# Kernel optimization log

Measured on AMD Instinct MI355X. Metric: run time of the kernel, lower is better.

The kernel has to match this reference:

```python
import jax, jax.numpy as jnp
import numpy as np
import math

INPUT_DIM = 1024
QUERY_DIM = 1024
VALUE_DIM = 1024

def setup_inputs() -> dict:
    key = jax.random.key(0)
    ks = jax.random.split(key, 7)
    N, T, D = 4, 4096, INPUT_DIM
    s_in = 1.0 / math.sqrt(D)
    X = jax.random.normal(ks[0], (N, T, D), dtype=jnp.float32)
    # torch.nn.Linear weights: (out, in), init ~ U(-1/sqrt(in), 1/sqrt(in))
    Wq = jax.random.uniform(ks[1], (QUERY_DIM, D), jnp.float32, -s_in, s_in)
    bq = jax.random.uniform(ks[2], (QUERY_DIM,), jnp.float32, -s_in, s_in)
    Wk = jax.random.uniform(ks[3], (QUERY_DIM, D), jnp.float32, -s_in, s_in)
    bk = jax.random.uniform(ks[4], (QUERY_DIM,), jnp.float32, -s_in, s_in)
    Wv = jax.random.uniform(ks[5], (VALUE_DIM, D), jnp.float32, -s_in, s_in)
    bv = jax.random.uniform(ks[6], (VALUE_DIM,), jnp.float32, -s_in, s_in)
    return {"X": X, "Wq": Wq, "bq": bq, "Wk": Wk, "bk": bk, "Wv": Wv, "bv": bv}

def reference(X, Wq, bq, Wk, bk, Wv, bv):
    N, T, D = X.shape
    q = jnp.einsum('ntd,qd->ntq', X, Wq) + bq  # (N,T,Q)
    k = jnp.einsum('ntd,qd->ntq', X, Wk) + bk  # (N,T,Q)
    v = jnp.einsum('ntd,vd->ntv', X, Wv) + bv  # (N,T,V)
    # NOTE: original scales by sqrt(D) = sqrt(input_dim), not sqrt(query_dim)
    scores = jnp.einsum('ntq,nsq->nts', q, k) / jnp.sqrt(jnp.asarray(D, X.dtype))
    attn = jax.nn.softmax(scores, axis=-1)  # (N,T,T)
    return jnp.einsum('nts,nsv->ntv', attn, v)
```

## Files before the change

kernel.cpp:

```cpp
#include <hip/hip_runtime.h>
#include <stdint.h>

typedef unsigned short u16;
typedef unsigned int u32;
typedef short shortx8 __attribute__((ext_vector_type(8)));
typedef float floatx4 __attribute__((ext_vector_type(4)));

__device__ __forceinline__ u16 f2bf(float f) {
    u32 u = __builtin_bit_cast(u32, f);
    u = (u + 0x7fffu + ((u >> 16) & 1u)) >> 16;
    return (u16)u;
}
__device__ __forceinline__ float bf2f(u16 h) {
    return __builtin_bit_cast(float, (u32)h << 16);
}

#if defined(__has_builtin)
#  if __has_builtin(__builtin_amdgcn_global_load_lds)
#    define HAVE_GLL 1
#  endif
#endif
#ifndef HAVE_GLL
#  define HAVE_GLL 0
#endif

#if HAVE_GLL
__device__ __forceinline__ void gload_lds16(const u16* g, u16* l) {
    __builtin_amdgcn_global_load_lds(
        (const __attribute__((address_space(1))) u32*)(const void*)g,
        (__attribute__((address_space(3))) u32*)(void*)l,
        16, 0, 0);
}
#endif

template <typename OutT, int MODE, int SWZ>
__global__ __launch_bounds__(256, 2) void gemm_bt(
    const u16* __restrict__ Ag, const u16* __restrict__ Bg, OutT* __restrict__ Cg,
    int lda, int ldb, int ldc, int K,
    const float* __restrict__ aux, float* __restrict__ sums, float scale,
    long long sAz, long long sBz, long long sCz, long long sXz,
    int swz_nhalf)
{
    __shared__ u16 smem[4][128 * 32];

    int z, mb, nb;
    if constexpr (SWZ) {
        const int f = blockIdx.x, xcd = f & 7, g = f >> 3;
        z = xcd >> 1;
        mb = g & 31;
        nb = (xcd & 1) * swz_nhalf + (g >> 5);
    } else {
        z = blockIdx.z; mb = blockIdx.y; nb = blockIdx.x;
    }
    const int m0 = mb * 128, n0 = nb * 128;

    const u16* A = Ag + (long long)z * sAz;
    const u16* B = Bg + (long long)z * sBz;
    OutT* C = Cg + (long long)z * sCz;
    const float* auxp = nullptr;
    if constexpr (MODE == 1 || MODE == 2 || MODE == 4)
        auxp = aux + (long long)z * sXz;
    float* sumz = nullptr;
    if constexpr (MODE == 3) sumz = sums + (long long)z * sXz;

    const int tid = threadIdx.x, lane = tid & 63, wv = tid >> 6;

    const int srow = lane >> 2;
    const int schunk = (lane & 3) * 8;
    const u16* gA0 = A + (size_t)(m0 + wv * 16 + srow) * lda + schunk;
    const u16* gA1 = gA0 + (size_t)64 * lda;
    const u16* gB0 = B + (size_t)(n0 + wv * 16 + srow) * ldb + schunk;
    const u16* gB1 = gB0 + (size_t)64 * ldb;
    const int wb = wv * 512;

    const int wm = (wv & 1) * 64, wn = (wv >> 1) * 64;
    const int mi = lane & 15, kq = lane >> 4;

    floatx4 acc[4][4] = {};

    for (int k0 = 0; k0 < K; k0 += 64) {
#if HAVE_GLL
        gload_lds16(gA0,      &smem[0][wb]);
        gload_lds16(gA1,      &smem[0][2048 + wb]);
        gload_lds16(gA0 + 32, &smem[1][wb]);
        gload_lds16(gA1 + 32, &smem[1][2048 + wb]);
        gload_lds16(gB0,      &smem[2][wb]);
        gload_lds16(gB1,      &smem[2][2048 + wb]);
        gload_lds16(gB0 + 32, &smem[3][wb]);
        gload_lds16(gB1 + 32, &smem[3][2048 + wb]);
#else
        *(shortx8*)(&smem[0][wb] + lane * 8)        = *(const shortx8*)gA0;
        *(shortx8*)(&smem[0][2048 + wb] + lane * 8) = *(const shortx8*)gA1;
        *(shortx8*)(&smem[1][wb] + lane * 8)        = *(const shortx8*)(gA0 + 32);
        *(shortx8*)(&smem[1][2048 + wb] + lane * 8) = *(const shortx8*)(gA1 + 32);
        *(shortx8*)(&smem[2][wb] + lane * 8)        = *(const shortx8*)gB0;
        *(shortx8*)(&smem[2][2048 + wb] + lane * 8) = *(const shortx8*)gB1;
        *(shortx8*)(&smem[3][wb] + lane * 8)        = *(const shortx8*)(gB0 + 32);
        *(shortx8*)(&smem[3][2048 + wb] + lane * 8) = *(const shortx8*)(gB1 + 32);
#endif
        gA0 += 64; gA1 += 64; gB0 += 64; gB1 += 64;
        __syncthreads();

#pragma unroll
        for (int h = 0; h < 2; h++) {
            const u16* Ap = smem[h];
            const u16* Bp = smem[2 + h];
            shortx8 af[4], bfr[4];
#pragma unroll
            for (int i = 0; i < 4; i++)
                af[i] = *(const shortx8*)(Ap + (wm + i * 16 + mi) * 32 + kq * 8);
#pragma unroll
            for (int j = 0; j < 4; j++)
                bfr[j] = *(const shortx8*)(Bp + (wn + j * 16 + mi) * 32 + kq * 8);
#pragma unroll
            for (int i = 0; i < 4; i++)
#pragma unroll
                for (int j = 0; j < 4; j++)
                    acc[i][j] = __builtin_amdgcn_mfma_f32_16x16x32_bf16(
                        af[i], bfr[j], acc[i][j], 0, 0, 0);
        }
        __syncthreads();
    }

    float cb[4];
    if constexpr (MODE == 1) {
#pragma unroll
        for (int j = 0; j < 4; j++) cb[j] = auxp[n0 + wn + j * 16 + mi];
    }

    if constexpr (sizeof(OutT) == 2) {
        u16* ct = &smem[0][0];
#pragma unroll
        for (int i = 0; i < 4; i++) {
#pragma unroll
            for (int r = 0; r < 4; r++) {
                const int lrow = wm + i * 16 + kq * 4 + r;
                float radd = 0.f;
                if constexpr (MODE == 2) radd = auxp[m0 + lrow];
                float rs = 0.f;
#pragma unroll
                for (int j = 0; j < 4; j++) {
                    float v = acc[i][j][r];
                    if constexpr (MODE == 1) v += cb[j];
                    if constexpr (MODE == 2) v += radd;
                    if constexpr (MODE == 3) { v = __expf(v * scale); rs += v; }
                    ct[lrow * 128 + wn + j * 16 + mi] = f2bf(v);
                }
                if constexpr (MODE == 3) {
                    rs += __shfl_xor(rs, 1);
                    rs += __shfl_xor(rs, 2);
                    rs += __shfl_xor(rs, 4);
                    rs += __shfl_xor(rs, 8);
                    if (mi == 0) atomicAdd(&sumz[m0 + lrow], rs);
                }
            }
        }
        __syncthreads();
#pragma unroll
        for (int it = 0; it < 8; it++) {
            const int fl = (it * 256 + tid) * 8;
            const int row = fl >> 7, col = fl & 127;
            *(uint4*)(C + (size_t)(m0 + row) * ldc + n0 + col) =
                *(const uint4*)(ct + fl);
        }
    } else {
#pragma unroll
        for (int i = 0; i < 4; i++) {
#pragma unroll
            for (int r = 0; r < 4; r++) {
                const int row = m0 + wm + i * 16 + kq * 4 + r;
                float rmul = 1.f;
                if constexpr (MODE == 4) rmul = 1.0f / auxp[row];
                OutT* crow = C + (size_t)row * ldc;
#pragma unroll
                for (int j = 0; j < 4; j++) {
                    const int col = n0 + wn + j * 16 + mi;
                    crow[col] = acc[i][j][r] * rmul;
                }
            }
        }
    }
}

__global__ __launch_bounds__(256) void cvt_bf16(const float* __restrict__ s,
                                                u16* __restrict__ d, int n8)
{
    int i = blockIdx.x * 256 + threadIdx.x;
    if (i >= n8) return;
    const float4* sp = (const float4*)s;
    float4 a = sp[2 * i], b = sp[2 * i + 1];
    uint4 o;
    o.x = (u32)f2bf(a.x) | ((u32)f2bf(a.y) << 16);
    o.y = (u32)f2bf(a.z) | ((u32)f2bf(a.w) << 16);
    o.z = (u32)f2bf(b.x) | ((u32)f2bf(b.y) << 16);
    o.w = (u32)f2bf(b.z) | ((u32)f2bf(b.w) << 16);
    *(uint4*)(d + 8 * i) = o;
}

__global__ void concat2(const float* __restrict__ a, const float* __restrict__ b,
                        float* __restrict__ d, int n)
{
    int i = blockIdx.x * 256 + threadIdx.x;
    if (i < n) d[i] = a[i];
    else if (i < 2 * n) d[i] = b[i - n];
}

extern "C" void kernel_launch(void* const* d_in, const int* in_sizes, int n_in,
                              void* d_out, int out_size, void* d_ws, size_t ws_size,
                              hipStream_t stream)
{
    const float* X  = (const float*)d_in[0];
    const float* Wq = (const float*)d_in[1];
    const float* bq = (const float*)d_in[2];
    const float* Wk = (const float*)d_in[3];
    const float* bk = (const float*)d_in[4];
    const float* Wv = (const float*)d_in[5];
    const float* bv = (const float*)d_in[6];
    float* out = (float*)d_out;

    const int T = 4096, NT = 4 * T;
    const long long TL = T;

    char* ws = (char*)d_ws;
    size_t off = 0;
    auto alloc = [&](size_t bytes) {
        char* p = ws + off;
        off += (bytes + 255) & ~(size_t)255;
        return p;
    };
    u16*   Wqk  = (u16*)alloc((size_t)2048 * 1024 * 2);
    u16*   Wvb  = (u16*)alloc((size_t)1024 * 1024 * 2);
    float* bqk  = (float*)alloc(2048 * 4);
    u16*   QK   = (u16*)alloc((size_t)NT * 2048 * 2);
    u16*   Vt   = (u16*)alloc((size_t)1024 * NT * 2);
    float* sums = (float*)alloc((size_t)NT * 4);
    size_t pbase = off;
    u16*   Xb   = (u16*)alloc((size_t)NT * 1024 * 2);
    u16*   P    = Xb;

    const size_t need_batched = pbase + (size_t)4 * T * T * 2;
    const bool batched = ws_size >= need_batched;

    cvt_bf16<<<dim3((NT * 1024 / 8 + 255) / 256), dim3(256), 0, stream>>>(X, Xb, NT * 1024 / 8);
    cvt_bf16<<<dim3(512), dim3(256), 0, stream>>>(Wq, Wqk, 1024 * 1024 / 8);
    cvt_bf16<<<dim3(512), dim3(256), 0, stream>>>(Wk, Wqk + 1024 * 1024, 1024 * 1024 / 8);
    cvt_bf16<<<dim3(512), dim3(256), 0, stream>>>(Wv, Wvb, 1024 * 1024 / 8);
    concat2<<<dim3(8), dim3(256), 0, stream>>>(bq, bk, bqk, 1024);
    hipMemsetAsync(sums, 0, (size_t)NT * 4, stream);

    gemm_bt<u16, 1, 0><<<dim3(16, 128, 1), dim3(256), 0, stream>>>(
        Xb, Wqk, QK, 1024, 1024, 2048, 1024, bqk, nullptr, 0.f, 0, 0, 0, 0, 0);

    gemm_bt<u16, 2, 0><<<dim3(128, 8, 1), dim3(256), 0, stream>>>(
        Wvb, Xb, Vt, 1024, 1024, NT, 1024, bv, nullptr, 0.f, 0, 0, 0, 0, 0);

    if (batched) {
        gemm_bt<u16, 3, 1><<<dim3(4096), dim3(256), 0, stream>>>(
            QK, QK + 1024, P, 2048, 2048, T, 1024, nullptr, sums, 0.03125f,
            TL * 2048, TL * 2048, TL * T, TL, 16);
        gemm_bt<float, 4, 1><<<dim3(1024), dim3(256), 0, stream>>>(
            P, Vt, out, T, NT, 1024, T, sums, nullptr, 0.f,
            TL * T, TL, TL * 1024, TL, 4);
    } else {
        for (int z = 0; z < 4; z++) {
            const u16* Qz = QK + (size_t)z * T * 2048;
            gemm_bt<u16, 3, 0><<<dim3(32, 32, 1), dim3(256), 0, stream>>>(
                Qz, Qz + 1024, P, 2048, 2048, T, 1024, nullptr, sums + (size_t)z * T,
                0.03125f, 0, 0, 0, 0, 0);
            gemm_bt<float, 4, 0><<<dim3(8, 32, 1), dim3(256), 0, stream>>>(
                P, Vt + (size_t)z * T, out + (size_t)z * T * 1024,
                T, NT, 1024, T, sums + (size_t)z * T, nullptr, 0.f, 0, 0, 0, 0, 0);
        }
    }
    (void)in_sizes; (void)n_in; (void)out_size;
}
```

Before: 582.5 us.

## Store Q/K projections as FP8 and compute attention scores with FP8 MFMA

The QK projection GEMM now writes FP8 (e4m3) output instead of bf16. A new dedicated scores kernel computes QK^T with the scaled 16x16x128 f8f6f4 MFMA, using 128-byte K tiles and an XOR-swizzled LDS layout, then applies exp and accumulates row sums. The generic bf16 GEMM also gains an XOR swizzle on its LDS chunks to reduce bank conflicts. The aim is to halve Q/K memory traffic and raise matrix throughput for the largest GEMM, at the cost of reduced precision in the attention logits.

Measured after the change: 929.2 us. +59.5%, slower.

```diff
diff --git a/kernel.cpp b/kernel.cpp
--- a/kernel.cpp
+++ b/kernel.cpp
@@ -2,33 +2,58 @@
 #include <stdint.h>
 
 typedef unsigned short u16;
+typedef unsigned char u8;
 typedef unsigned int u32;
 typedef short shortx8 __attribute__((ext_vector_type(8)));
 typedef float floatx4 __attribute__((ext_vector_type(4)));
+typedef int intx4 __attribute__((ext_vector_type(4)));
+typedef int intx8 __attribute__((ext_vector_type(8)));
 
 __device__ __forceinline__ u16 f2bf(float f) {
     u32 u = __builtin_bit_cast(u32, f);
     u = (u + 0x7fffu + ((u >> 16) & 1u)) >> 16;
     return (u16)u;
 }
-__device__ __forceinline__ float bf2f(u16 h) {
-    return __builtin_bit_cast(float, (u32)h << 16);
-}
 
 #if defined(__has_builtin)
+#  if __has_builtin(__builtin_amdgcn_cvt_pk_fp8_f32)
+#    define HAVE_CVT_FP8 1
+#  endif
 #  if __has_builtin(__builtin_amdgcn_global_load_lds)
 #    define HAVE_GLL 1
 #  endif
 #endif
+#ifndef HAVE_CVT_FP8
+#  define HAVE_CVT_FP8 0
+#endif
 #ifndef HAVE_GLL
 #  define HAVE_GLL 0
 #endif
 
+__device__ __forceinline__ u8 f2fp8(float f) {
+#if HAVE_CVT_FP8
+    return (u8)(__builtin_amdgcn_cvt_pk_fp8_f32(f, f, 0, false) & 0xff);
+#else
+    u32 u = __builtin_bit_cast(u32, f);
+    u32 s = (u >> 24) & 0x80u;
+    u32 m = u & 0x7fffffffu;
+    if (m >= 0x43e00000u) return (u8)(s | 0x7eu);
+    if (m < 0x3c800000u) {
+        int q = __float2int_rn(__builtin_bit_cast(float, m) * 512.f);
+        return (u8)(s | (u32)q);
+    }
+    u32 r = m + 0x7ffffu + ((m >> 20) & 1u);
+    u32 code = (((r >> 23) - 120u) << 3) | ((r >> 20) & 7u);
+    if (code > 0x7eu) code = 0x7eu;
+    return (u8)(s | code);
+#endif
+}
+
 #if HAVE_GLL
-__device__ __forceinline__ void gload_lds16(const u16* g, u16* l) {
+__device__ __forceinline__ void gload_lds16(const void* g, void* l) {
     __builtin_amdgcn_global_load_lds(
-        (const __attribute__((address_space(1))) u32*)(const void*)g,
-        (__attribute__((address_space(3))) u32*)(void*)l,
+        (const __attribute__((address_space(1))) u32*)g,
+        (__attribute__((address_space(3))) u32*)l,
         16, 0, 0);
 }
 #endif
@@ -37,7 +62,7 @@
 __global__ __launch_bounds__(256, 2) void gemm_bt(
     const u16* __restrict__ Ag, const u16* __restrict__ Bg, OutT* __restrict__ Cg,
     int lda, int ldb, int ldc, int K,
-    const float* __restrict__ aux, float* __restrict__ sums, float scale,
+    const float* __restrict__ aux, float scale,
     long long sAz, long long sBz, long long sCz, long long sXz,
     int swz_nhalf)
 {
@@ -57,24 +82,21 @@
     const u16* A = Ag + (long long)z * sAz;
     const u16* B = Bg + (long long)z * sBz;
     OutT* C = Cg + (long long)z * sCz;
-    const float* auxp = nullptr;
-    if constexpr (MODE == 1 || MODE == 2 || MODE == 4)
-        auxp = aux + (long long)z * sXz;
-    float* sumz = nullptr;
-    if constexpr (MODE == 3) sumz = sums + (long long)z * sXz;
+    const float* auxp = aux ? aux + (long long)z * sXz : nullptr;
 
     const int tid = threadIdx.x, lane = tid & 63, wv = tid >> 6;
 
     const int srow = lane >> 2;
-    const int schunk = (lane & 3) * 8;
-    const u16* gA0 = A + (size_t)(m0 + wv * 16 + srow) * lda + schunk;
+    const int sch  = ((lane & 3) ^ (srow & 3)) * 8;
+    const u16* gA0 = A + (size_t)(m0 + wv * 16 + srow) * lda + sch;
     const u16* gA1 = gA0 + (size_t)64 * lda;
-    const u16* gB0 = B + (size_t)(n0 + wv * 16 + srow) * ldb + schunk;
+    const u16* gB0 = B + (size_t)(n0 + wv * 16 + srow) * ldb + sch;
     const u16* gB1 = gB0 + (size_t)64 * ldb;
     const int wb = wv * 512;
 
     const int wm = (wv & 1) * 64, wn = (wv >> 1) * 64;
     const int mi = lane & 15, kq = lane >> 4;
+    const int xm = mi & 3;
 
     floatx4 acc[4][4] = {};
 
@@ -108,10 +130,10 @@
             shortx8 af[4], bfr[4];
 #pragma unroll
             for (int i = 0; i < 4; i++)
-                af[i] = *(const shortx8*)(Ap + (wm + i * 16 + mi) * 32 + kq * 8);
+                af[i] = *(const shortx8*)(Ap + (wm + i * 16 + mi) * 32 + (kq ^ xm) * 8);
 #pragma unroll
             for (int j = 0; j < 4; j++)
-                bfr[j] = *(const shortx8*)(Bp + (wn + j * 16 + mi) * 32 + kq * 8);
+                bfr[j] = *(const shortx8*)(Bp + (wn + j * 16 + mi) * 32 + (kq ^ xm) * 8);
 #pragma unroll
             for (int i = 0; i < 4; i++)
 #pragma unroll
@@ -137,21 +159,12 @@
                 const int lrow = wm + i * 16 + kq * 4 + r;
                 float radd = 0.f;
                 if constexpr (MODE == 2) radd = auxp[m0 + lrow];
-                float rs = 0.f;
 #pragma unroll
                 for (int j = 0; j < 4; j++) {
                     float v = acc[i][j][r];
                     if constexpr (MODE == 1) v += cb[j];
                     if constexpr (MODE == 2) v += radd;
-                    if constexpr (MODE == 3) { v = __expf(v * scale); rs += v; }
                     ct[lrow * 128 + wn + j * 16 + mi] = f2bf(v);
-                }
-                if constexpr (MODE == 3) {
-                    rs += __shfl_xor(rs, 1);
-                    rs += __shfl_xor(rs, 2);
-                    rs += __shfl_xor(rs, 4);
-                    rs += __shfl_xor(rs, 8);
-                    if (mi == 0) atomicAdd(&sumz[m0 + lrow], rs);
                 }
             }
         }
@@ -163,6 +176,29 @@
             *(uint4*)(C + (size_t)(m0 + row) * ldc + n0 + col) =
                 *(const uint4*)(ct + fl);
         }
+    } else if constexpr (sizeof(OutT) == 1) {
+        u8* ct = (u8*)&smem[0][0];
+#pragma unroll
+        for (int i = 0; i < 4; i++) {
+#pragma unroll
+            for (int r = 0; r < 4; r++) {
+                const int lrow = wm + i * 16 + kq * 4 + r;
+#pragma unroll
+                for (int j = 0; j < 4; j++) {
+                    float v = acc[i][j][r];
+                    if constexpr (MODE == 1) v += cb[j];
+                    ct[lrow * 128 + wn + j * 16 + mi] = f2fp8(v);
+                }
+            }
+        }
+        __syncthreads();
+#pragma unroll
+        for (int it = 0; it < 4; it++) {
+            const int fl = (it * 256 + tid) * 16;
+            const int row = fl >> 7, col = fl & 127;
+            *(uint4*)(C + (size_t)(m0 + row) * ldc + n0 + col) =
+                *(const uint4*)(ct + fl);
+        }
     } else {
 #pragma unroll
         for (int i = 0; i < 4; i++) {
@@ -179,6 +215,117 @@
                 }
             }
         }
+    }
+}
+
+template <int SWZ>
+__global__ __launch_bounds__(256, 2) void gemm_fp8_scores(
+    const u8* __restrict__ Qg, const u8* __restrict__ Kg, u16* __restrict__ Pg,
+    float* __restrict__ sums, float scale, int T)
+{
+    __shared__ u8 smem[2][128 * 128];
+
+    int z, mb, nb;
+    if constexpr (SWZ) {
+        const int f = blockIdx.x, xcd = f & 7, g = f >> 3;
+        z = xcd >> 1;
+        mb = g & 31;
+        nb = (xcd & 1) * 16 + (g >> 5);
+    } else {
+        z = blockIdx.z; mb = blockIdx.y; nb = blockIdx.x;
+    }
+    const int m0 = mb * 128, n0 = nb * 128;
+
+    const u8* A = Qg + (size_t)z * T * 2048;
+    const u8* B = Kg + (size_t)z * T * 2048;
+    u16* P = Pg + (size_t)z * T * T;
+    float* sumz = sums + (size_t)z * T;
+
+    const int tid = threadIdx.x, lane = tid & 63, wv = tid >> 6;
+
+    const int srow = lane >> 3;
+    const int sch  = ((lane & 7) ^ srow) * 16;
+    const u8* gA = A + (size_t)(m0 + wv * 32 + srow) * 2048 + sch;
+    const u8* gB = B + (size_t)(n0 + wv * 32 + srow) * 2048 + sch;
+    u8* lA = &smem[0][wv * 4096];
+    u8* lB = &smem[1][wv * 4096];
+
+    const int wm = (wv & 1) * 64, wn = (wv >> 1) * 64;
+    const int mi = lane & 15, kq = lane >> 4;
+    const int xm = mi & 7;
+
+    floatx4 acc[4][4] = {};
+
+    for (int k0 = 0; k0 < 1024; k0 += 128) {
+#if HAVE_GLL
+#pragma unroll
+        for (int i = 0; i < 4; i++) {
+            gload_lds16(gA + (size_t)i * 8 * 2048, lA + i * 1024);
+            gload_lds16(gB + (size_t)i * 8 * 2048, lB + i * 1024);
+        }
+#else
+#pragma unroll
+        for (int i = 0; i < 4; i++) {
+            *(uint4*)(lA + i * 1024 + lane * 16) = *(const uint4*)(gA + (size_t)i * 8 * 2048);
+            *(uint4*)(lB + i * 1024 + lane * 16) = *(const uint4*)(gB + (size_t)i * 8 * 2048);
+        }
+#endif
+        gA += 128; gB += 128;
+        __syncthreads();
+
+        intx8 af[4], bfr[4];
+#pragma unroll
+        for (int i = 0; i < 4; i++) {
+            const u8* p = &smem[0][(wm + i * 16 + mi) * 128];
+            union { intx8 v8; intx4 v4[2]; } u;
+            u.v4[0] = *(const intx4*)(p + (((2 * kq) ^ xm) * 16));
+            u.v4[1] = *(const intx4*)(p + (((2 * kq + 1) ^ xm) * 16));
+            af[i] = u.v8;
+        }
+#pragma unroll
+        for (int j = 0; j < 4; j++) {
+            const u8* p = &smem[1][(wn + j * 16 + mi) * 128];
+            union { intx8 v8; intx4 v4[2]; } u;
+            u.v4[0] = *(const intx4*)(p + (((2 * kq) ^ xm) * 16));
+            u.v4[1] = *(const intx4*)(p + (((2 * kq + 1) ^ xm) * 16));
+            bfr[j] = u.v8;
+        }
+#pragma unroll
+        for (int i = 0; i < 4; i++)
+#pragma unroll
+            for (int j = 0; j < 4; j++)
+                acc[i][j] = __builtin_amdgcn_mfma_scale_f32_16x16x128_f8f6f4(
+                    af[i], bfr[j], acc[i][j], 0, 0,
+                    0, 0x7f7f7f7f, 0, 0x7f7f7f7f);
+        __syncthreads();
+    }
+
+    u16* ct = (u16*)&smem[0][0];
+#pragma unroll
+    for (int i = 0; i < 4; i++) {
+#pragma unroll
+        for (int r = 0; r < 4; r++) {
+            const int lrow = wm + i * 16 + kq * 4 + r;
+            float rs = 0.f;
+#pragma unroll
+            for (int j = 0; j < 4; j++) {
+                float v = __expf(acc[i][j][r] * scale);
+                rs += v;
+                ct[lrow * 128 + wn + j * 16 + mi] = f2bf(v);
+            }
+            rs += __shfl_xor(rs, 1);
+            rs += __shfl_xor(rs, 2);
+            rs += __shfl_xor(rs, 4);
+            rs += __shfl_xor(rs, 8);
+            if (mi == 0) atomicAdd(&sumz[m0 + lrow], rs);
+        }
+    }
+    __syncthreads();
+#pragma unroll
+    for (int it = 0; it < 8; it++) {
+        const int fl = (it * 256 + tid) * 8;
+        const int row = fl >> 7, col = fl & 127;
+        *(uint4*)(P + (size_t)(m0 + row) * T + n0 + col) = *(const uint4*)(ct + fl);
     }
 }
 
@@ -231,7 +378,7 @@
     u16*   Wqk  = (u16*)alloc((size_t)2048 * 1024 * 2);
     u16*   Wvb  = (u16*)alloc((size_t)1024 * 1024 * 2);
     float* bqk  = (float*)alloc(2048 * 4);
-    u16*   QK   = (u16*)alloc((size_t)NT * 2048 * 2);
+    u8*    QK   = (u8*)alloc((size_t)NT * 2048);
     u16*   Vt   = (u16*)alloc((size_t)1024 * NT * 2);
     float* sums = (float*)alloc((size_t)NT * 4);
     size_t pbase = off;
@@ -248,28 +395,26 @@
     concat2<<<dim3(8), dim3(256), 0, stream>>>(bq, bk, bqk, 1024);
     hipMemsetAsync(sums, 0, (size_t)NT * 4, stream);
 
-    gemm_bt<u16, 1, 0><<<dim3(16, 128, 1), dim3(256), 0, stream>>>(
-        Xb, Wqk, QK, 1024, 1024, 2048, 1024, bqk, nullptr, 0.f, 0, 0, 0, 0, 0);
+    gemm_bt<u8, 1, 0><<<dim3(16, 128, 1), dim3(256), 0, stream>>>(
+        Xb, Wqk, QK, 1024, 1024, 2048, 1024, bqk, 0.f, 0, 0, 0, 0, 0);
 
     gemm_bt<u16, 2, 0><<<dim3(128, 8, 1), dim3(256), 0, stream>>>(
-        Wvb, Xb, Vt, 1024, 1024, NT, 1024, bv, nullptr, 0.f, 0, 0, 0, 0, 0);
+        Wvb, Xb, Vt, 1024, 1024, NT, 1024, bv, 0.f, 0, 0, 0, 0, 0);
 
     if (batched) {
-        gemm_bt<u16, 3, 1><<<dim3(4096), dim3(256), 0, stream>>>(
-            QK, QK + 1024, P, 2048, 2048, T, 1024, nullptr, sums, 0.03125f,
-            TL * 2048, TL * 2048, TL * T, TL, 16);
+        gemm_fp8_scores<1><<<dim3(4096), dim3(256), 0, stream>>>(
+            QK, QK + 1024, P, sums, 0.03125f, T);
         gemm_bt<float, 4, 1><<<dim3(1024), dim3(256), 0, stream>>>(
-            P, Vt, out, T, NT, 1024, T, sums, nullptr, 0.f,
+            P, Vt, out, T, NT, 1024, T, sums, 0.f,
             TL * T, TL, TL * 1024, TL, 4);
     } else {
         for (int z = 0; z < 4; z++) {
-            const u16* Qz = QK + (size_t)z * T * 2048;
-            gemm_bt<u16, 3, 0><<<dim3(32, 32, 1), dim3(256), 0, stream>>>(
-                Qz, Qz + 1024, P, 2048, 2048, T, 1024, nullptr, sums + (size_t)z * T,
-                0.03125f, 0, 0, 0, 0, 0);
+            const u8* Qz = QK + (size_t)z * T * 2048;
+            gemm_fp8_scores<0><<<dim3(32, 32, 1), dim3(256), 0, stream>>>(
+                Qz, Qz + 1024, P - (size_t)0, sums + (size_t)z * T - (size_t)0, 0.03125f, T);
             gemm_bt<float, 4, 0><<<dim3(8, 32, 1), dim3(256), 0, stream>>>(
                 P, Vt + (size_t)z * T, out + (size_t)z * T * 1024,
-                T, NT, 1024, T, sums + (size_t)z * T, nullptr, 0.f, 0, 0, 0, 0, 0);
+                T, NT, 1024, T, sums + (size_t)z * T, 0.f, 0, 0, 0, 0, 0);
         }
     }
     (void)in_sizes; (void)n_in; (void)out_size;
```
